# Optimization experiments

Measured on AMD Instinct MI355X. Metric: run time of the kernel, lower is better.

The kernel has to match this reference:

```python
import jax, jax.numpy as jnp
import numpy as np

B, N, H = 8, 2048, 256

def setup_inputs() -> dict:
    key = jax.random.key(0)
    k1, k2, k3, k4, k5 = jax.random.split(key, 5)
    h = jax.random.normal(k1, (B, N, H), dtype=jnp.float32)
    node_mask = jnp.ones((B, N, 1), dtype=jnp.float32)
    n_nodes = N  # unused by the forward math, kept for signature fidelity
    s1 = 1.0 / np.sqrt(H)
    W1 = jax.random.uniform(k2, (H, H), minval=-s1, maxval=s1, dtype=jnp.float32)
    b1 = jax.random.uniform(k3, (H,), minval=-s1, maxval=s1, dtype=jnp.float32)
    w2 = jax.random.uniform(k4, (H,), minval=-s1, maxval=s1, dtype=jnp.float32)
    b2 = jax.random.uniform(k5, (), minval=-s1, maxval=s1, dtype=jnp.float32)
    return {"h": h, "node_mask": node_mask, "n_nodes": n_nodes,
            "W1": W1, "b1": b1, "w2": w2, "b2": b2}

def reference(h, node_mask, n_nodes, W1, b1, w2, b2):
    # node_dec: Linear + SiLU
    x = jax.nn.silu(jnp.einsum('bnh,oh->bno', h, W1) + b1)  # [B,N,H]
    # pre_di applied to pairwise difference is linear, so factor:
    # pre_di(x_i - x_j) = (x_i @ w2) - (x_j @ w2) + b2
    s = jnp.einsum('bnh,h->bn', x, w2)                       # [B,N]
    out = s[:, :, None] - s[:, None, :] + b2                 # [B,N,N]
    return out.astype(jnp.int64)                             # torch .long() truncates
```

## Files before the change

kernel.cpp:

```cpp
#include <hip/hip_runtime.h>
#include <math.h>

#define B_ 8
#define N_ 2048
#define H_ 256

__global__ __launch_bounds__(256)
void transpose_w1(const float* __restrict__ W1, float* __restrict__ W1T) {
    W1T[(size_t)blockIdx.x * H_ + threadIdx.x] =
        W1[(size_t)threadIdx.x * H_ + blockIdx.x];
}

__global__ __launch_bounds__(256)
__attribute__((amdgpu_waves_per_eu(2, 4)))
void s_kernel(const float* __restrict__ hp, const float* __restrict__ W1T,
              const float* __restrict__ b1, const float* __restrict__ w2,
              double* __restrict__ s_out) {
    __shared__ double hs[16][H_];

    const int t = threadIdx.x;
    const int m0 = blockIdx.x * 16;

    #pragma unroll
    for (int i = 0; i < 16; ++i)
        hs[i][t] = (double)hp[(size_t)(m0 + i) * H_ + t];
    __syncthreads();

    const int lane = t & 63;
    const int wave = t >> 6;
    const int r0 = wave * 4;
    const int o0 = lane * 4;

    const float* wp = W1T + o0;

    double acc[4][4];
    #pragma unroll
    for (int j = 0; j < 4; ++j)
        #pragma unroll
        for (int r = 0; r < 4; ++r) acc[j][r] = 0.0;

    float4 wcur[4], wnxt[4];
    double2 hA[4], hB[4];

    #pragma unroll
    for (int kk = 0; kk < 4; ++kk)
        wcur[kk] = *reinterpret_cast<const float4*>(wp + (size_t)kk * H_);
    #pragma unroll
    for (int r = 0; r < 4; ++r)
        hA[r] = *reinterpret_cast<const double2*>(&hs[r0 + r][0]);

    #define PAIR(hv, wka, wkb)                                                \
        do {                                                                  \
            const double a0 = (double)wka.x, a1 = (double)wka.y,              \
                         a2 = (double)wka.z, a3 = (double)wka.w;              \
            const double c0 = (double)wkb.x, c1 = (double)wkb.y,              \
                         c2 = (double)wkb.z, c3 = (double)wkb.w;              \
            _Pragma("unroll")                                                 \
            for (int r = 0; r < 4; ++r) {                                     \
                acc[0][r] = fma(a0, hv[r].x, acc[0][r]);                      \
                acc[0][r] = fma(c0, hv[r].y, acc[0][r]);                      \
                acc[1][r] = fma(a1, hv[r].x, acc[1][r]);                      \
                acc[1][r] = fma(c1, hv[r].y, acc[1][r]);                      \
                acc[2][r] = fma(a2, hv[r].x, acc[2][r]);                      \
                acc[2][r] = fma(c2, hv[r].y, acc[2][r]);                      \
                acc[3][r] = fma(a3, hv[r].x, acc[3][r]);                      \
                acc[3][r] = fma(c3, hv[r].y, acc[3][r]);                      \
            }                                                                 \
        } while (0)

    for (int kc = 0; kc < H_; kc += 4) {
        const int kn = (kc + 4 < H_) ? (kc + 4) : 0;
        #pragma unroll
        for (int kk = 0; kk < 4; ++kk)
            wnxt[kk] = *reinterpret_cast<const float4*>(
                wp + (size_t)(kn + kk) * H_);
        #pragma unroll
        for (int r = 0; r < 4; ++r)
            hB[r] = *reinterpret_cast<const double2*>(&hs[r0 + r][kc + 2]);
        PAIR(hA, wcur[0], wcur[1]);
        #pragma unroll
        for (int r = 0; r < 4; ++r)
            hA[r] = *reinterpret_cast<const double2*>(&hs[r0 + r][kn]);
        PAIR(hB, wcur[2], wcur[3]);
        #pragma unroll
        for (int kk = 0; kk < 4; ++kk) wcur[kk] = wnxt[kk];
    }
    #undef PAIR

    const float4 b1v = *reinterpret_cast<const float4*>(b1 + o0);
    const float4 w2v = *reinterpret_cast<const float4*>(w2 + o0);
    double psum[4] = {0.0, 0.0, 0.0, 0.0};
    #define EPI(j, bc, wc)                                                    \
        do {                                                                  \
            const double bb = (double)bc, ww = (double)wc;                    \
            _Pragma("unroll")                                                 \
            for (int r = 0; r < 4; ++r) {                                     \
                const double u = acc[j][r] + bb;                              \
                psum[r] += ww * (u / (1.0 + exp(-u)));                        \
            }                                                                 \
        } while (0)
    EPI(0, b1v.x, w2v.x);
    EPI(1, b1v.y, w2v.y);
    EPI(2, b1v.z, w2v.z);
    EPI(3, b1v.w, w2v.w);
    #undef EPI

    #pragma unroll
    for (int r = 0; r < 4; ++r) {
        double v = psum[r];
        v += __shfl_xor(v, 1, 64);
        v += __shfl_xor(v, 2, 64);
        v += __shfl_xor(v, 4, 64);
        v += __shfl_xor(v, 8, 64);
        v += __shfl_xor(v, 16, 64);
        v += __shfl_xor(v, 32, 64);
        if (lane == 0) s_out[m0 + r0 + r] = v;
    }
}

__global__ __launch_bounds__(256)
void pair_kernel(const double* __restrict__ s, const float* __restrict__ b2p,
                 int* __restrict__ out) {
    const double b2 = (double)b2p[0];
    const unsigned total4 = (unsigned)(B_) * (unsigned)(N_) * (unsigned)(N_) / 4u;
    const unsigned stride = gridDim.x * blockDim.x;
    for (unsigned idx = blockIdx.x * blockDim.x + threadIdx.x; idx < total4;
         idx += stride) {
        const unsigned base = idx * 4u;
        const unsigned bi  = base >> 22;
        const unsigned rem = base & ((1u << 22) - 1u);
        const unsigned i   = rem >> 11;
        const unsigned j   = rem & (N_ - 1u);
        const double si = s[bi * N_ + i];
        const double* sp = s + bi * N_ + j;
        const double sj0 = sp[0], sj1 = sp[1], sj2 = sp[2], sj3 = sp[3];
        int4 o;
        o.x = (int)trunc((si - sj0) + b2);
        o.y = (int)trunc((si - sj1) + b2);
        o.z = (int)trunc((si - sj2) + b2);
        o.w = (int)trunc((si - sj3) + b2);
        *reinterpret_cast<int4*>(out + base) = o;
    }
}

extern "C" void kernel_launch(void* const* d_in, const int* in_sizes, int n_in,
                              void* d_out, int out_size, void* d_ws, size_t ws_size,
                              hipStream_t stream) {
    const float* hp = (const float*)d_in[0];
    const float* W1 = (const float*)d_in[3];
    const float* b1 = (const float*)d_in[4];
    const float* w2 = (const float*)d_in[5];
    const float* b2 = (const float*)d_in[6];

    float* W1T = (float*)d_ws;
    double* s  = (double*)((char*)d_ws + H_ * H_ * sizeof(float));
    int* out = (int*)d_out;

    transpose_w1<<<H_, H_, 0, stream>>>(W1, W1T);
    s_kernel<<<(B_ * N_) / 16, 256, 0, stream>>>(hp, W1T, b1, w2, s);
    pair_kernel<<<2048, 256, 0, stream>>>(s, b2, out);
}
```

Baseline: 86.84 us.

## Drop LDS staging of h; load h rows directly via wave-uniform scalar loads

Removes the shared-memory double copy of the h tile and the block barrier. Each wave now reads its own 4 rows of h straight from global memory, with the row index made wave-uniform via readfirstlane so the loads can become scalar loads. The k loop is deepened to 8-wide double-buffered chunks of W1T and h. This cuts LDS traffic and the sync, but adds register pressure from two 32-float h buffers and two 8-float4 W buffers on top of the double accumulators.

```diff
diff --git a/kernel.cpp b/kernel.cpp
--- a/kernel.cpp
+++ b/kernel.cpp
@@ -16,21 +16,13 @@
 void s_kernel(const float* __restrict__ hp, const float* __restrict__ W1T,
               const float* __restrict__ b1, const float* __restrict__ w2,
               double* __restrict__ s_out) {
-    __shared__ double hs[16][H_];
-
     const int t = threadIdx.x;
-    const int m0 = blockIdx.x * 16;
-
-    #pragma unroll
-    for (int i = 0; i < 16; ++i)
-        hs[i][t] = (double)hp[(size_t)(m0 + i) * H_ + t];
-    __syncthreads();
-
     const int lane = t & 63;
-    const int wave = t >> 6;
-    const int r0 = wave * 4;
+    const int wave = __builtin_amdgcn_readfirstlane(t >> 6);
+    const int m0 = blockIdx.x * 16 + wave * 4;
     const int o0 = lane * 4;
 
+    const float* hr = hp + (size_t)m0 * H_;
     const float* wp = W1T + o0;
 
     double acc[4][4];
@@ -39,53 +31,72 @@
         #pragma unroll
         for (int r = 0; r < 4; ++r) acc[j][r] = 0.0;
 
-    float4 wcur[4], wnxt[4];
-    double2 hA[4], hB[4];
+    float4 wA[8], wB[8];
+    float hA[32], hB[32];
 
-    #pragma unroll
-    for (int kk = 0; kk < 4; ++kk)
-        wcur[kk] = *reinterpret_cast<const float4*>(wp + (size_t)kk * H_);
-    #pragma unroll
-    for (int r = 0; r < 4; ++r)
-        hA[r] = *reinterpret_cast<const double2*>(&hs[r0 + r][0]);
+    #define LOADW(dst, kcv)                                                   \
+        do {                                                                  \
+            _Pragma("unroll")                                                 \
+            for (int kk = 0; kk < 8; ++kk)                                    \
+                dst[kk] = *reinterpret_cast<const float4*>(                   \
+                    wp + (size_t)((kcv) + kk) * H_);                          \
+        } while (0)
 
-    #define PAIR(hv, wka, wkb)                                                \
+    #define LOADH(dst, kcv)                                                   \
         do {                                                                  \
-            const double a0 = (double)wka.x, a1 = (double)wka.y,              \
-                         a2 = (double)wka.z, a3 = (double)wka.w;              \
-            const double c0 = (double)wkb.x, c1 = (double)wkb.y,              \
-                         c2 = (double)wkb.z, c3 = (double)wkb.w;              \
             _Pragma("unroll")                                                 \
-            for (int r = 0; r < 4; ++r) {                                     \
-                acc[0][r] = fma(a0, hv[r].x, acc[0][r]);                      \
-                acc[0][r] = fma(c0, hv[r].y, acc[0][r]);                      \
-                acc[1][r] = fma(a1, hv[r].x, acc[1][r]);                      \
-                acc[1][r] = fma(c1, hv[r].y, acc[1][r]);                      \
-                acc[2][r] = fma(a2, hv[r].x, acc[2][r]);                      \
-                acc[2][r] = fma(c2, hv[r].y, acc[2][r]);                      \
-                acc[3][r] = fma(a3, hv[r].x, acc[3][r]);                      \
-                acc[3][r] = fma(c3, hv[r].y, acc[3][r]);                      \
+            for (int r = 0; r < 4; ++r)                                       \
+                _Pragma("unroll")                                             \
+                for (int kk = 0; kk < 8; ++kk)                                \
+                    dst[r * 8 + kk] = hr[r * H_ + (kcv) + kk];                \
+        } while (0)
+
+    #define COMPUTE(wv, hbuf)                                                 \
+        do {                                                                  \
+            _Pragma("unroll")                                                 \
+            for (int kk = 0; kk < 8; ++kk) {                                  \
+                const double h0 = (double)hbuf[0 * 8 + kk];                   \
+                const double h1 = (double)hbuf[1 * 8 + kk];                   \
+                const double h2 = (double)hbuf[2 * 8 + kk];                   \
+                const double h3 = (double)hbuf[3 * 8 + kk];                   \
+                const double a0 = (double)wv[kk].x;                           \
+                const double a1 = (double)wv[kk].y;                           \
+                const double a2 = (double)wv[kk].z;                           \
+                const double a3 = (double)wv[kk].w;                           \
+                acc[0][0] = fma(a0, h0, acc[0][0]);                           \
+                acc[0][1] = fma(a0, h1, acc[0][1]);                           \
+                acc[0][2] = fma(a0, h2, acc[0][2]);                           \
+                acc[0][3] = fma(a0, h3, acc[0][3]);                           \
+                acc[1][0] = fma(a1, h0, acc[1][0]);                           \
+                acc[1][1] = fma(a1, h1, acc[1][1]);                           \
+                acc[1][2] = fma(a1, h2, acc[1][2]);                           \
+                acc[1][3] = fma(a1, h3, acc[1][3]);                           \
+                acc[2][0] = fma(a2, h0, acc[2][0]);                           \
+                acc[2][1] = fma(a2, h1, acc[2][1]);                           \
+                acc[2][2] = fma(a2, h2, acc[2][2]);                           \
+                acc[2][3] = fma(a2, h3, acc[2][3]);                           \
+                acc[3][0] = fma(a3, h0, acc[3][0]);                           \
+                acc[3][1] = fma(a3, h1, acc[3][1]);                           \
+                acc[3][2] = fma(a3, h2, acc[3][2]);                           \
+                acc[3][3] = fma(a3, h3, acc[3][3]);                           \
             }                                                                 \
         } while (0)
 
-    for (int kc = 0; kc < H_; kc += 4) {
-        const int kn = (kc + 4 < H_) ? (kc + 4) : 0;
-        #pragma unroll
-        for (int kk = 0; kk < 4; ++kk)
-            wnxt[kk] = *reinterpret_cast<const float4*>(
-                wp + (size_t)(kn + kk) * H_);
-        #pragma unroll
-        for (int r = 0; r < 4; ++r)
-            hB[r] = *reinterpret_cast<const double2*>(&hs[r0 + r][kc + 2]);
-        PAIR(hA, wcur[0], wcur[1]);
-        #pragma unroll
-        for (int r = 0; r < 4; ++r)
-            hA[r] = *reinterpret_cast<const double2*>(&hs[r0 + r][kn]);
-        PAIR(hB, wcur[2], wcur[3]);
-        #pragma unroll
-        for (int kk = 0; kk < 4; ++kk) wcur[kk] = wnxt[kk];
+    LOADW(wA, 0);
+    LOADH(hA, 0);
+    for (int kc = 0; kc < H_; kc += 16) {
+        LOADW(wB, kc + 8);
+        LOADH(hB, kc + 8);
+        COMPUTE(wA, hA);
+        if (kc + 16 < H_) {
+            LOADW(wA, kc + 16);
+            LOADH(hA, kc + 16);
+        }
+        COMPUTE(wB, hB);
     }
-    #undef PAIR
+    #undef LOADW
+    #undef LOADH
+    #undef COMPUTE
 
     const float4 b1v = *reinterpret_cast<const float4*>(b1 + o0);
     const float4 w2v = *reinterpret_cast<const float4*>(w2 + o0);
@@ -114,7 +125,7 @@
         v += __shfl_xor(v, 8, 64);
         v += __shfl_xor(v, 16, 64);
         v += __shfl_xor(v, 32, 64);
-        if (lane == 0) s_out[m0 + r0 + r] = v;
+        if (lane == 0) s_out[m0 + r] = v;
     }
 }
 
```

After: 94.29 us. +8.6%, slower.
